# Optimization experiments

Measured on AMD Instinct MI355X. Metric: run time of the kernel, lower is better.

Reference implementation:

```python
import jax, jax.numpy as jnp
import numpy as np

B, S, D = 2, 1024, 4096          # batch, prefill seqlen, model dim
H, KVH, HD = 32, 8, 128          # q heads, kv heads, head dim
MAX = 2048                       # kv-cache capacity
THETA = 1000000.0
REP = H // KVH


def _rope_tables(pos):
    # pos: [S] int -> cos/sin [S, HD]
    inv_freq = 1.0 / (THETA ** (jnp.arange(0, HD, 2, dtype=jnp.float32) / HD))
    freqs = pos[:, None].astype(jnp.float32) * inv_freq[None, :]
    emb = jnp.concatenate([freqs, freqs], axis=-1)
    return jnp.cos(emb), jnp.sin(emb)


def _rotate_half(t):
    t1, t2 = jnp.split(t, 2, axis=-1)
    return jnp.concatenate([-t2, t1], axis=-1)


def setup_inputs() -> dict:
    key = jax.random.key(0)
    k = jax.random.split(key, 8)
    sc = 1.0 / np.sqrt(D)
    x = jax.random.normal(k[0], (B, S, D), jnp.float32)
    storage_idx = jnp.arange(S, dtype=jnp.int32)
    cache = jnp.zeros((2, 1, B, KVH, MAX, HD), jnp.float32)
    causal = jnp.tril(jnp.ones((MAX, MAX), bool))
    mask = jnp.where(causal, 0.0, -1e9).astype(jnp.float32)
    Wq = jax.random.normal(k[1], (D, H * HD), jnp.float32) * sc
    bq = jax.random.normal(k[2], (H * HD,), jnp.float32) * 0.01
    Wk = jax.random.normal(k[3], (D, KVH * HD), jnp.float32) * sc
    bk = jax.random.normal(k[4], (KVH * HD,), jnp.float32) * 0.01
    Wv = jax.random.normal(k[5], (D, KVH * HD), jnp.float32) * sc
    bv = jax.random.normal(k[6], (KVH * HD,), jnp.float32) * 0.01
    Wo = jax.random.normal(k[7], (H * HD, D), jnp.float32) * sc
    return {"x": x, "storage_idx": storage_idx, "cache": cache, "mask": mask,
            "Wq": Wq, "bq": bq, "Wk": Wk, "bk": bk, "Wv": Wv, "bv": bv, "Wo": Wo}


def reference(x, storage_idx, cache, mask, Wq, bq, Wk, bk, Wv, bv, Wo):
    bsz, seqlen, _ = x.shape
    # QKV projections -> [b, heads, s, hd]
    xq = (x @ Wq + bq).reshape(bsz, seqlen, H, HD).transpose(0, 2, 1, 3)
    xk = (x @ Wk + bk).reshape(bsz, seqlen, KVH, HD).transpose(0, 2, 1, 3)
    xv = (x @ Wv + bv).reshape(bsz, seqlen, KVH, HD).transpose(0, 2, 1, 3)
    # inline RoPE at positions storage_idx
    cos, sin = _rope_tables(storage_idx)       # [s, hd]
    cos = cos[None, None]                      # [1,1,s,hd]
    sin = sin[None, None]
    xq = xq * cos + _rotate_half(xq) * sin
    xk = xk * cos + _rotate_half(xk) * sin
    # KV-cache scatter (index_copy_ on dim -2 at storage_idx)
    keys = cache[0, 0].at[:, :, storage_idx, :].set(xk)    # [b, kvh, MAX, hd]
    values = cache[1, 0].at[:, :, storage_idx, :].set(xv)
    # GQA: repeat kv heads
    keys = jnp.repeat(keys, REP, axis=1)       # [b, H, MAX, hd]
    values = jnp.repeat(values, REP, axis=1)
    # attention with additive mask rows gathered at storage_idx
    scores = jnp.einsum('bhqd,bhkd->bhqk', xq, keys) / np.sqrt(HD)
    scores = scores + mask[storage_idx][None, None]        # [b, H, s, MAX]
    attn = jax.nn.softmax(scores, axis=-1)
    out = jnp.einsum('bhqk,bhkd->bhqd', attn, values)
    out = out.transpose(0, 2, 1, 3).reshape(bsz, seqlen, H * HD)
    return out @ Wo
```

## Files before the change

### kernel.cpp

```cpp
#include <hip/hip_runtime.h>
#include <hip/hip_bf16.h>

typedef unsigned short u16;
typedef unsigned int   u32;
using bf16x8 = __attribute__((ext_vector_type(8))) short;
using f32x4  = __attribute__((ext_vector_type(4))) float;

#define AS1 __attribute__((address_space(1)))
#define AS3 __attribute__((address_space(3)))

static constexpr int S_   = 1024;
static constexpr int D_   = 4096;
static constexpr int H_   = 32;
static constexpr int KVH_ = 8;
static constexpr int HD_  = 128;
static constexpr int NQKV = H_*HD_ + 2*KVH_*HD_;

__device__ __forceinline__ u16 f2bf(float f) {
  union { float f; u32 u; } v; v.f = f;
  u32 r = v.u + 0x7FFFu + ((v.u >> 16) & 1u);
  return (u16)(r >> 16);
}

__global__ void k_convert(const float* __restrict__ src, u16* __restrict__ dst, int n4) {
  int i = blockIdx.x * blockDim.x + threadIdx.x;
  if (i >= n4) return;
  float4 v = ((const float4*)src)[i];
  ushort4 o;
  o.x = f2bf(v.x); o.y = f2bf(v.y); o.z = f2bf(v.z); o.w = f2bf(v.w);
  ((ushort4*)dst)[i] = o;
}

__global__ __launch_bounds__(256) void k_transpose_w(
    const float* __restrict__ src, u16* __restrict__ dst, int K, int N) {
  __shared__ float t[64][65];
  int k0 = blockIdx.y * 64, n0 = blockIdx.x * 64;
  int tid = threadIdx.x;
  int lr = tid >> 4;
  int lc = (tid & 15) * 4;
#pragma unroll
  for (int i = 0; i < 4; ++i) {
    float4 v = *(const float4*)&src[(size_t)(k0 + lr + i*16) * N + n0 + lc];
    t[lc+0][lr + i*16] = v.x;
    t[lc+1][lr + i*16] = v.y;
    t[lc+2][lr + i*16] = v.z;
    t[lc+3][lr + i*16] = v.w;
  }
  __syncthreads();
  int wn = tid >> 3;
  int wk = (tid & 7) * 8;
#pragma unroll
  for (int i = 0; i < 2; ++i) {
    const float* row = &t[wn + i*32][wk];
    ushort4 a, b;
    a.x = f2bf(row[0]); a.y = f2bf(row[1]); a.z = f2bf(row[2]); a.w = f2bf(row[3]);
    b.x = f2bf(row[4]); b.y = f2bf(row[5]); b.z = f2bf(row[6]); b.w = f2bf(row[7]);
    u16* o = &dst[(size_t)(n0 + wn + i*32) * K + k0 + wk];
    *(ushort4*)o = a;
    *(ushort4*)(o + 4) = b;
  }
}

__global__ void k_transpose_v(const u16* __restrict__ src, u16* __restrict__ dst) {
  __shared__ u16 t[32][33];
  int bg = blockIdx.z;
  int s0 = blockIdx.x * 32, h0 = blockIdx.y * 32;
  src += (size_t)bg * S_ * HD_;
  dst += (size_t)bg * S_ * HD_;
  int tx = threadIdx.x, ty = threadIdx.y;
#pragma unroll
  for (int i = 0; i < 4; ++i)
    t[ty + i*8][tx] = src[(size_t)(s0 + ty + i*8) * HD_ + h0 + tx];
  __syncthreads();
#pragma unroll
  for (int i = 0; i < 4; ++i)
    dst[(size_t)(h0 + ty + i*8) * S_ + s0 + tx] = t[tx][ty + i*8];
}

__global__ void k_rope(const int* __restrict__ sidx, float* __restrict__ cosd,
                       float* __restrict__ sind) {
  int i = blockIdx.x * blockDim.x + threadIdx.x;
  int s = i >> 6, d = i & 63;
  float pos  = (float)sidx[s];
  float invf = expf(-0.21586735246819178f * (float)d);
  float ph   = pos * invf;
  cosd[i] = cosf(ph);
  sind[i] = sinf(ph);
}

#define BAR   __builtin_amdgcn_s_barrier()
#define SCHB  __builtin_amdgcn_sched_barrier(0)

__global__ __launch_bounds__(512, 2) void k_gemmq(
    const u16* __restrict__ A, const u16* __restrict__ Bt,
    const float* __restrict__ bq, const float* __restrict__ bk,
    const float* __restrict__ bv,
    const float* __restrict__ cosd, const float* __restrict__ sind,
    u16* __restrict__ qb, u16* __restrict__ kb, u16* __restrict__ vb)
{
  constexpr int K = 4096;
  constexpr int ABYT = 256*128, BBYT = 256*128, STEP = ABYT+BBYT;
  __shared__ __align__(16) char lds[2*STEP];

  const int cpx = (int)gridDim.x >> 3;
  const int wkid = ((int)blockIdx.x & 7)*cpx + ((int)blockIdx.x >> 3);
  const int NT = 24;
  const int m0 = (wkid / NT) * 256, n0 = (wkid % NT) * 256;
  const int tid = threadIdx.x, w = tid>>6, lane = tid&63;
  const int l15 = lane&15, l4 = lane>>4;
  const int wr = w>>1, wc = w&1;
  const int row0 = tid>>3;
  const int ss = (tid&7) ^ (row0&7);
  const int NK = K >> 6;

  f32x4 acc[4][8];
#pragma unroll
  for (int i = 0; i < 4; ++i)
#pragma unroll
    for (int j = 0; j < 8; ++j) acc[i][j] = (f32x4){0.f,0.f,0.f,0.f};

  bf16x8 af[2][2][2];
  bf16x8 bfr[2][4][2];

#define QCHUNK(kt_, part_, r0c_)                                              \
  __builtin_amdgcn_global_load_lds(                                           \
    (AS1 void*)(((part_) ? Bt + (size_t)(n0 + (r0c_) + row0)*K                \
                         : A  + (size_t)(m0 + (r0c_) + row0)*K)               \
                + (size_t)(kt_)*64 + ss*8),                                   \
    (AS3 void*)(lds + ((kt_)&1)*STEP + (part_)*ABYT + (r0c_)*128 + w*1024),   \
    16, 0, 0)

#define QR_A(mh_, lA_)                                                        \
  _Pragma("unroll") for (int i2 = 0; i2 < 2; ++i2)                            \
  _Pragma("unroll") for (int kk = 0; kk < 2; ++kk) {                          \
    int row = wr*64 + ((mh_)*2 + i2)*16 + l15;                                \
    af[mh_][i2][kk] = *(const bf16x8*)((lA_) + row*128 + (((kk*4+l4) ^ (row&7)) << 4)); }

#define QR_B(nh_, lB_)                                                        \
  _Pragma("unroll") for (int jj = 0; jj < 4; ++jj)                            \
  _Pragma("unroll") for (int kk = 0; kk < 2; ++kk) {                          \
    int row = wc*128 + ((nh_)*4 + jj)*16 + l15;                               \
    bfr[nh_][jj][kk] = *(const bf16x8*)((lB_) + row*128 + (((kk*4+l4) ^ (row&7)) << 4)); }

#define QMFMA(mh_, nh_)                                                       \
  __builtin_amdgcn_s_setprio(1);                                              \
  _Pragma("unroll") for (int i2 = 0; i2 < 2; ++i2)                            \
  _Pragma("unroll") for (int jj = 0; jj < 4; ++jj)                            \
  _Pragma("unroll") for (int kk = 0; kk < 2; ++kk)                            \
    acc[(mh_)*2+i2][(nh_)*4+jj] = __builtin_amdgcn_mfma_f32_16x16x32_bf16(    \
        af[mh_][i2][kk], bfr[nh_][jj][kk], acc[(mh_)*2+i2][(nh_)*4+jj], 0, 0, 0); \
  __builtin_amdgcn_s_setprio(0);

  QCHUNK(0,0,0); QCHUNK(0,0,64); QCHUNK(0,0,128); QCHUNK(0,0,192);
  QCHUNK(0,1,0); QCHUNK(0,1,64); QCHUNK(0,1,128); QCHUNK(0,1,192);
  QCHUNK(1,0,0); QCHUNK(1,0,64); QCHUNK(1,0,128); QCHUNK(1,0,192);
  QCHUNK(1,1,0); QCHUNK(1,1,64); QCHUNK(1,1,128); QCHUNK(1,1,192);
  asm volatile("s_waitcnt vmcnt(8)" ::: "memory");
  BAR; SCHB;
  {
    const char* lA0 = lds;
    const char* lB0 = lds + ABYT;
    QR_A(0, lA0); QR_B(0, lB0);
  }

  for (int kt = 0; kt < NK; ++kt) {
    const char* lA = lds + (kt&1)*STEP;
    const char* lB = lA + ABYT;
    QR_B(1, lB);
    asm volatile("s_waitcnt lgkmcnt(8)" ::: "memory");
    SCHB;
    QMFMA(0,0);
    QR_A(1, lA);
    asm volatile("s_waitcnt lgkmcnt(4)" ::: "memory");
    BAR; SCHB;
    if (kt+2 < NK) { QCHUNK(kt+2,1,0); QCHUNK(kt+2,1,64); QCHUNK(kt+2,1,128); QCHUNK(kt+2,1,192); }
    QMFMA(0,1);
    asm volatile("s_waitcnt lgkmcnt(0)" ::: "memory");
    BAR; SCHB;
    if (kt+2 < NK) { QCHUNK(kt+2,0,0); QCHUNK(kt+2,0,64); QCHUNK(kt+2,0,128); QCHUNK(kt+2,0,192); }
    QMFMA(1,0);
    if (kt+1 < NK) {
      if (kt+2 < NK) asm volatile("s_waitcnt vmcnt(8)" ::: "memory");
      else           asm volatile("s_waitcnt vmcnt(0)" ::: "memory");
      BAR; SCHB;
      const char* lAn = lds + ((kt+1)&1)*STEP;
      const char* lBn = lAn + ABYT;
      QR_A(0, lAn); QR_B(0, lBn);
      SCHB;
    }
    QMFMA(1,1);
  }
#undef QCHUNK
#undef QR_A
#undef QR_B
#undef QMFMA

  const int btype = (n0 >= H_*HD_) + (n0 >= H_*HD_ + KVH_*HD_);
  const int colbase = n0 + wc*128 - (btype==1 ? H_*HD_ : btype==2 ? H_*HD_+KVH_*HD_ : 0);
  const int hloc = colbase >> 7;
  const float* bias = btype==0 ? bq : btype==1 ? bk : bv;
  u16* dst = btype==0 ? qb : btype==1 ? kb : vb;
  const int nheads = btype==0 ? H_ : KVH_;
  const float scale = btype==0 ? 0.08838834764831845f : 1.0f;

  float bb[8];
#pragma unroll
  for (int j = 0; j < 8; ++j) bb[j] = bias[colbase + j*16 + l15];

#pragma unroll
  for (int i = 0; i < 4; ++i)
#pragma unroll
    for (int r = 0; r < 4; ++r) {
      int sr = m0 + wr*64 + i*16 + l4*4 + r;
      int b_ = sr >> 10, s_ = sr & 1023;
      size_t obase = (((size_t)b_*nheads + hloc)*S_ + s_)*(size_t)HD_;
      if (btype < 2) {
#pragma unroll
        for (int j = 0; j < 4; ++j) {
          float cs = cosd[s_*64 + j*16 + l15];
          float sn = sind[s_*64 + j*16 + l15];
          float lo = acc[i][j][r]   + bb[j];
          float hi = acc[i][j+4][r] + bb[j+4];
          dst[obase + j*16 + l15]      = f2bf((lo*cs - hi*sn) * scale);
          dst[obase + 64 + j*16 + l15] = f2bf((hi*cs + lo*sn) * scale);
        }
      } else {
#pragma unroll
        for (int j = 0; j < 8; ++j)
          dst[obase + j*16 + l15] = f2bf(acc[i][j][r] + bb[j]);
      }
    }
}

__global__ __launch_bounds__(512, 2) void k_gemmo(
    const u16* __restrict__ A, const u16* __restrict__ Bt,
    float* __restrict__ C, int N, int K)
{
  constexpr int ABYT = 128*128, BBYT = 256*128, STEP = ABYT+BBYT;
  __shared__ __align__(16) char lds[2*STEP];

  const int cpx = (int)gridDim.x >> 3;
  const int wkid = ((int)blockIdx.x & 7)*cpx + ((int)blockIdx.x >> 3);
  const int NT = N / 256;
  const int m0 = (wkid / NT) * 128, n0 = (wkid % NT) * 256;
  const int tid = threadIdx.x, w = tid>>6, lane = tid&63;
  const int l15 = lane&15, l4 = lane>>4;
  const int wr = w>>2, wc = w&3;
  const int row0 = tid>>3;
  const int ss = (tid&7) ^ (row0&7);
  const int NK = K >> 6;

  f32x4 acc[4][4];
#pragma unroll
  for (int i = 0; i < 4; ++i)
#pragma unroll
    for (int j = 0; j < 4; ++j) acc[i][j] = (f32x4){0.f,0.f,0.f,0.f};

  bf16x8 af[2][2][2];
  bf16x8 bfr[2][2][2];

#define OCHUNK(kt_, part_, r0c_)                                              \
  __builtin_amdgcn_global_load_lds(                                           \
    (AS1 void*)(((part_) ? Bt + (size_t)(n0 + (r0c_) + row0)*K                \
                         : A  + (size_t)(m0 + (r0c_) + row0)*K)               \
                + (size_t)(kt_)*64 + ss*8),                                   \
    (AS3 void*)(lds + ((kt_)&1)*STEP + (part_)*ABYT + (r0c_)*128 + w*1024),   \
    16, 0, 0)

#define OR_A(mh_, lA_)                                                        \
  _Pragma("unroll") for (int i2 = 0; i2 < 2; ++i2)                            \
  _Pragma("unroll") for (int kk = 0; kk < 2; ++kk) {                          \
    int row = wr*64 + ((mh_)*2 + i2)*16 + l15;                                \
    af[mh_][i2][kk] = *(const bf16x8*)((lA_) + row*128 + (((kk*4+l4) ^ (row&7)) << 4)); }

#define OR_B(nh_, lB_)                                                        \
  _Pragma("unroll") for (int j2 = 0; j2 < 2; ++j2)                            \
  _Pragma("unroll") for (int kk = 0; kk < 2; ++kk) {                          \
    int row = wc*64 + ((nh_)*2 + j2)*16 + l15;                                \
    bfr[nh_][j2][kk] = *(const bf16x8*)((lB_) + row*128 + (((kk*4+l4) ^ (row&7)) << 4)); }

#define OMFMA(mh_, nh_)                                                       \
  __builtin_amdgcn_s_setprio(1);                                              \
  _Pragma("unroll") for (int i2 = 0; i2 < 2; ++i2)                            \
  _Pragma("unroll") for (int j2 = 0; j2 < 2; ++j2)                            \
  _Pragma("unroll") for (int kk = 0; kk < 2; ++kk)                            \
    acc[(mh_)*2+i2][(nh_)*2+j2] = __builtin_amdgcn_mfma_f32_16x16x32_bf16(    \
        af[mh_][i2][kk], bfr[nh_][j2][kk], acc[(mh_)*2+i2][(nh_)*2+j2], 0, 0, 0); \
  __builtin_amdgcn_s_setprio(0);

  OCHUNK(0,0,0); OCHUNK(0,0,64);
  OCHUNK(0,1,0); OCHUNK(0,1,64); OCHUNK(0,1,128); OCHUNK(0,1,192);
  OCHUNK(1,0,0); OCHUNK(1,0,64);
  OCHUNK(1,1,0); OCHUNK(1,1,64); OCHUNK(1,1,128); OCHUNK(1,1,192);
  asm volatile("s_waitcnt vmcnt(6)" ::: "memory");
  BAR; SCHB;
  {
    const char* lA0 = lds;
    const char* lB0 = lds + ABYT;
    OR_A(0, lA0); OR_B(0, lB0);
  }

  for (int kt = 0; kt < NK; ++kt) {
    const char* lA = lds + (kt&1)*STEP;
    const char* lB = lA + ABYT;
    OR_B(1, lB);
    asm volatile("s_waitcnt lgkmcnt(4)" ::: "memory");
    SCHB;
    OMFMA(0,0);
    OR_A(1, lA);
    asm volatile("s_waitcnt lgkmcnt(4)" ::: "memory");
    BAR; SCHB;
    if (kt+2 < NK) { OCHUNK(kt+2,1,0); OCHUNK(kt+2,1,64); OCHUNK(kt+2,1,128); OCHUNK(kt+2,1,192); }
    OMFMA(0,1);
    asm volatile("s_waitcnt lgkmcnt(0)" ::: "memory");
    BAR; SCHB;
    if (kt+2 < NK) { OCHUNK(kt+2,0,0); OCHUNK(kt+2,0,64); }
    OMFMA(1,0);
    if (kt+1 < NK) {
      if (kt+2 < NK) asm volatile("s_waitcnt vmcnt(6)" ::: "memory");
      else           asm volatile("s_waitcnt vmcnt(0)" ::: "memory");
      BAR; SCHB;
      const char* lAn = lds + ((kt+1)&1)*STEP;
      const char* lBn = lAn + ABYT;
      OR_A(0, lAn); OR_B(0, lBn);
      SCHB;
    }
    OMFMA(1,1);
  }
#undef OCHUNK
#undef OR_A
#undef OR_B
#undef OMFMA

#pragma unroll
  for (int i = 0; i < 4; ++i)
#pragma unroll
    for (int j = 0; j < 4; ++j) {
      int r0 = m0 + wr*64 + i*16 + l4*4;
      int c0 = n0 + wc*64 + j*16 + l15;
#pragma unroll
      for (int r = 0; r < 4; ++r)
        C[(size_t)(r0 + r) * N + c0] = acc[i][j][r];
    }
}

__global__ __launch_bounds__(256, 4) void k_attn(
    const u16* __restrict__ Q, const u16* __restrict__ Kc,
    const u16* __restrict__ Vt, u16* __restrict__ AO)
{
  __shared__ __align__(16) char Kls[2][16384];
  __shared__ __align__(16) char Vls[2][16384];
  __shared__ u16 Pl[4][1024];

  int id = blockIdx.x;
  int slot = id >> 3;
  int bg   = (id & 7)*2 + (slot & 1);
  int rem  = slot >> 1;
  int h_in = rem & 3, bx = rem >> 2;
  int b = bg >> 3, g = bg & 7, h = g*4 + h_in;
  int tA = bx, tB = 15 - bx;

  int tid = threadIdx.x, w = tid >> 6, lane = tid & 63;
  int l15 = lane & 15, l4 = lane >> 4;
  const u16* Qh = Q  + ((size_t)b*H_   + h) * S_ * HD_;
  const u16* Kp = Kc + ((size_t)b*KVH_ + g) * S_ * HD_;
  const u16* Vp = Vt + ((size_t)b*KVH_ + g) * (size_t)HD_ * S_;
  u16* AOh = AO + ((size_t)b*S_) * (H_*HD_) + h*HD_;
  char* Pw = (char*)&Pl[w][0];

  int kOff[4], vOff[4];
#pragma unroll
  for (int c = 0; c < 4; ++c) {
    int ci = c*256 + tid;
    int krow = ci >> 4, ks = ci & 15;
    kOff[c] = krow * HD_ + ((ks & 8) | ((ks & 7) ^ (krow & 7))) * 8;
    int vrow = ci >> 3, vs = ci & 7;
    vOff[c] = vrow * S_ + (vs ^ (vrow & 7)) * 8;
  }

#define ASTAGE(kv_, bb_) {                                                    \
    const u16* ks_ = Kp + (size_t)(kv_) * 64 * HD_;                           \
    const u16* vs_ = Vp + (size_t)(kv_) * 64;                                 \
    _Pragma("unroll") for (int c = 0; c < 4; ++c) {                           \
      __builtin_amdgcn_global_load_lds((AS1 void*)(ks_ + kOff[c]),            \
          (AS3 void*)(&Kls[bb_][0] + c*4096 + w*1024), 16, 0, 0);             \
      __builtin_amdgcn_global_load_lds((AS1 void*)(vs_ + vOff[c]),            \
          (AS3 void*)(&Vls[bb_][0] + c*4096 + w*1024), 16, 0, 0); } }

  bf16x8 qf[4];
#pragma unroll
  for (int kc = 0; kc < 4; ++kc)
    qf[kc] = *(const bf16x8*)(Qh + (size_t)(tA*64 + w*16 + l15)*HD_ + kc*32 + l4*8);

  f32x4 o[8];
#pragma unroll
  for (int n = 0; n < 8; ++n) o[n] = (f32x4){0.f,0.f,0.f,0.f};
  float mrow[4] = {-3e38f,-3e38f,-3e38f,-3e38f};
  float lrow[4] = {0.f,0.f,0.f,0.f};

  ASTAGE(0, 0);
  asm volatile("s_waitcnt vmcnt(0)" ::: "memory");
  __builtin_amdgcn_s_barrier();

  const int NIT = tA + tB + 2;
  int buf = 0;
  for (int it = 0; it < NIT; ++it) {
    bool phA = (it <= tA);
    int kv = phA ? it : it - tA - 1;
    int qt = phA ? tA : tB;
    if (it + 1 < NIT) {
      int kvn = (it + 1 <= tA) ? it + 1 : it - tA;
      ASTAGE(kvn, buf ^ 1);
    }
    const char* Ksb = &Kls[buf][0];
    const char* Vsb = &Vls[buf][0];

    f32x4 sc[4];
    __builtin_amdgcn_s_setprio(1);
#pragma unroll
    for (int ct = 0; ct < 4; ++ct) {
      f32x4 s4 = (f32x4){0.f,0.f,0.f,0.f};
#pragma unroll
      for (int kc = 0; kc < 4; ++kc) {
        int row = ct*16 + l15, s = kc*4 + l4;
        bf16x8 kf = *(const bf16x8*)(Ksb + row*256 + ((((s & 7) ^ (row & 7)) | (s & 8)) << 4));
        s4 = __builtin_amdgcn_mfma_f32_16x16x32_bf16(qf[kc], kf, s4, 0, 0, 0);
      }
      sc[ct] = s4;
    }
    __builtin_amdgcn_s_setprio(0);

    if (kv == qt) {
      int qrow0 = qt*64 + w*16;
#pragma unroll
      for (int ct = 0; ct < 4; ++ct)
#pragma unroll
        for (int r = 0; r < 4; ++r) {
          int col = kv*64 + ct*16 + l15;
          if (col > qrow0 + l4*4 + r) sc[ct][r] = -1e9f;
        }
    }

    float f[4];
#pragma unroll
    for (int r = 0; r < 4; ++r) {
      float mx = fmaxf(fmaxf(sc[0][r], sc[1][r]), fmaxf(sc[2][r], sc[3][r]));
      mx = fmaxf(mx, __shfl_xor(mx, 1));
      mx = fmaxf(mx, __shfl_xor(mx, 2));
      mx = fmaxf(mx, __shfl_xor(mx, 4));
      mx = fmaxf(mx, __shfl_xor(mx, 8));
      float nm = fmaxf(mrow[r], mx);
      f[r] = __expf(mrow[r] - nm);
      mrow[r] = nm;
    }
    float rs[4] = {0.f,0.f,0.f,0.f};
#pragma unroll
    for (int ct = 0; ct < 4; ++ct)
#pragma unroll
      for (int r = 0; r < 4; ++r) {
        float p = __expf(sc[ct][r] - mrow[r]);
        rs[r] += p;
        int row = l4*4 + r, col = ct*16 + l15;
        int byte = row*128 + (((col >> 3) ^ (row & 7)) << 4) + (col & 7)*2;
        *(u16*)(Pw + byte) = f2bf(p);
      }
#pragma unroll
    for (int r = 0; r < 4; ++r) {
      float sum = rs[r];
      sum += __shfl_xor(sum, 1);
      sum += __shfl_xor(sum, 2);
      sum += __shfl_xor(sum, 4);
      sum += __shfl_xor(sum, 8);
      lrow[r] = lrow[r]*f[r] + sum;
    }
#pragma unroll
    for (int n = 0; n < 8; ++n)
#pragma unroll
      for (int r = 0; r < 4; ++r) o[n][r] *= f[r];

    __builtin_amdgcn_s_setprio(1);
#pragma unroll
    for (int kk = 0; kk < 2; ++kk) {
      int pbyte = l15*128 + (((kk*4 + l4) ^ (l15 & 7)) << 4);
      bf16x8 pf = *(const bf16x8*)(Pw + pbyte);
#pragma unroll
      for (int n = 0; n < 8; ++n) {
        int vrow = n*16 + l15, s = kk*4 + l4;
        bf16x8 vf = *(const bf16x8*)(Vsb + vrow*128 + ((s ^ (vrow & 7)) << 4));
        o[n] = __builtin_amdgcn_mfma_f32_16x16x32_bf16(pf, vf, o[n], 0, 0, 0);
      }
    }
    __builtin_amdgcn_s_setprio(0);

    if (it == tA) {
#pragma unroll
      for (int n = 0; n < 8; ++n)
#pragma unroll
        for (int r = 0; r < 4; ++r) {
          int srow = tA*64 + w*16 + l4*4 + r;
          AOh[(size_t)srow * (H_*HD_) + n*16 + l15] = f2bf(o[n][r] / lrow[r]);
        }
#pragma unroll
      for (int n = 0; n < 8; ++n) o[n] = (f32x4){0.f,0.f,0.f,0.f};
#pragma unroll
      for (int r = 0; r < 4; ++r) { mrow[r] = -3e38f; lrow[r] = 0.f; }
#pragma unroll
      for (int kc = 0; kc < 4; ++kc)
        qf[kc] = *(const bf16x8*)(Qh + (size_t)(tB*64 + w*16 + l15)*HD_ + kc*32 + l4*8);
    }

    asm volatile("s_waitcnt vmcnt(0)" ::: "memory");
    __builtin_amdgcn_s_barrier();
    buf ^= 1;
  }
#undef ASTAGE

#pragma unroll
  for (int n = 0; n < 8; ++n)
#pragma unroll
    for (int r = 0; r < 4; ++r) {
      int srow = tB*64 + w*16 + l4*4 + r;
      AOh[(size_t)srow * (H_*HD_) + n*16 + l15] = f2bf(o[n][r] / lrow[r]);
    }
}

extern "C" void kernel_launch(void* const* d_in, const int* in_sizes, int n_in,
                              void* d_out, int out_size, void* d_ws, size_t ws_size,
                              hipStream_t stream) {
  (void)in_sizes; (void)n_in; (void)out_size; (void)ws_size;
  const float* x   = (const float*)d_in[0];
  const int*   sid = (const int*)  d_in[1];
  const float* Wq  = (const float*)d_in[4];
  const float* bq  = (const float*)d_in[5];
  const float* Wk  = (const float*)d_in[6];
  const float* bk  = (const float*)d_in[7];
  const float* Wv  = (const float*)d_in[8];
  const float* bv  = (const float*)d_in[9];
  const float* Wo  = (const float*)d_in[10];
  float* out = (float*)d_out;

  char* ws = (char*)d_ws;
  u16*   xb   = (u16*)  (ws);
  u16*   WB   = (u16*)  (ws + 16777216);
  u16*   WoT  = (u16*)  (ws + 67108864);
  u16*   qb   = (u16*)  (ws + 150994944);
  u16*   kb   = (u16*)  (ws + 167772160);
  u16*   vb   = (u16*)  (ws + 171966464);
  u16*   VT   = (u16*)  (ws + 176160768);
  float* cosd = (float*)(ws + 180355072);
  float* sind = (float*)(ws + 180617216);
  u16*   AO   = xb;

  dim3 tb(32, 8);
  k_convert<<<8192, 256, 0, stream>>>(x, xb, (2048*4096)/4);
  k_transpose_w<<<dim3(64,64), 256, 0, stream>>>(Wq, WB, 4096, 4096);
  k_transpose_w<<<dim3(16,64), 256, 0, stream>>>(Wk, WB + (size_t)4096*4096, 4096, 1024);
  k_transpose_w<<<dim3(16,64), 256, 0, stream>>>(Wv, WB + (size_t)5120*4096, 4096, 1024);
  k_transpose_w<<<dim3(64,64), 256, 0, stream>>>(Wo, WoT, 4096, 4096);
  k_rope<<<256, 256, 0, stream>>>(sid, cosd, sind);
  k_gemmq<<<192, 512, 0, stream>>>(xb, WB, bq, bk, bv, cosd, sind, qb, kb, vb);
  k_transpose_v<<<dim3(32,4,16), tb, 0, stream>>>(vb, VT);
  k_attn<<<512, 256, 0, stream>>>(qb, kb, VT, AO);
  k_gemmo<<<256, 512, 0, stream>>>(AO, WoT, out, 4096, 4096);
}
```

Baseline: 286.4 us.

## Use 32x32x16 MFMA in output GEMM and merge weight transposes into one launch

The output projection GEMM switches from 16x16x32 bf16 MFMA tiles to 32x32x16 tiles. Each wave now holds four 32x32 accumulators instead of sixteen 16x16 ones, and the LDS fragment reads and output write indexing change to match. Separately, the four weight-transpose launches are merged into one kernel that routes by block index, which cuts launch overhead and tail gaps. The larger MFMA shape issues fewer instructions and reuses operands better, but it changes the LDS read pattern and could add bank conflicts or shift register pressure.

```diff
diff --git a/kernel.cpp b/kernel.cpp
--- a/kernel.cpp
+++ b/kernel.cpp
@@ -5,6 +5,7 @@
 typedef unsigned int   u32;
 using bf16x8 = __attribute__((ext_vector_type(8))) short;
 using f32x4  = __attribute__((ext_vector_type(4))) float;
+using f32x16 = __attribute__((ext_vector_type(16))) float;
 
 #define AS1 __attribute__((address_space(1)))
 #define AS3 __attribute__((address_space(3)))
@@ -31,10 +32,19 @@
   ((ushort4*)dst)[i] = o;
 }
 
-__global__ __launch_bounds__(256) void k_transpose_w(
-    const float* __restrict__ src, u16* __restrict__ dst, int K, int N) {
+__global__ __launch_bounds__(256) void k_transpose_all(
+    const float* __restrict__ Wq, const float* __restrict__ Wk,
+    const float* __restrict__ Wv, const float* __restrict__ Wo,
+    u16* __restrict__ WB, u16* __restrict__ WoT) {
+  constexpr int K = 4096;
   __shared__ float t[64][65];
-  int k0 = blockIdx.y * 64, n0 = blockIdx.x * 64;
+  int id = blockIdx.x;
+  const float* src; u16* dst; int N, tx, ty;
+  if (id < 4096)      { src = Wq; dst = WB;                        N = 4096; tx = id & 63; ty = id >> 6; }
+  else if (id < 5120) { id -= 4096; src = Wk; dst = WB + (size_t)4096*K; N = 1024; tx = id & 15; ty = id >> 4; }
+  else if (id < 6144) { id -= 5120; src = Wv; dst = WB + (size_t)5120*K; N = 1024; tx = id & 15; ty = id >> 4; }
+  else                { id -= 6144; src = Wo; dst = WoT;           N = 4096; tx = id & 63; ty = id >> 6; }
+  int k0 = ty * 64, n0 = tx * 64;
   int tid = threadIdx.x;
   int lr = tid >> 4;
   int lc = (tid & 15) * 4;
@@ -244,20 +254,16 @@
   const int NT = N / 256;
   const int m0 = (wkid / NT) * 128, n0 = (wkid % NT) * 256;
   const int tid = threadIdx.x, w = tid>>6, lane = tid&63;
-  const int l15 = lane&15, l4 = lane>>4;
+  const int l31 = lane & 31, lh = lane >> 5;
   const int wr = w>>2, wc = w&3;
   const int row0 = tid>>3;
   const int ss = (tid&7) ^ (row0&7);
   const int NK = K >> 6;
 
-  f32x4 acc[4][4];
-#pragma unroll
-  for (int i = 0; i < 4; ++i)
-#pragma unroll
-    for (int j = 0; j < 4; ++j) acc[i][j] = (f32x4){0.f,0.f,0.f,0.f};
-
-  bf16x8 af[2][2][2];
-  bf16x8 bfr[2][2][2];
+  f32x16 acc00 = {}, acc01 = {}, acc10 = {}, acc11 = {};
+
+  bf16x8 af[2][4];
+  bf16x8 bfr[2][4];
 
 #define OCHUNK(kt_, part_, r0c_)                                              \
   __builtin_amdgcn_global_load_lds(                                           \
@@ -268,24 +274,19 @@
     16, 0, 0)
 
 #define OR_A(mh_, lA_)                                                        \
-  _Pragma("unroll") for (int i2 = 0; i2 < 2; ++i2)                            \
-  _Pragma("unroll") for (int kk = 0; kk < 2; ++kk) {                          \
-    int row = wr*64 + ((mh_)*2 + i2)*16 + l15;                                \
-    af[mh_][i2][kk] = *(const bf16x8*)((lA_) + row*128 + (((kk*4+l4) ^ (row&7)) << 4)); }
+  _Pragma("unroll") for (int st = 0; st < 4; ++st) {                          \
+    int row = wr*64 + (mh_)*32 + l31;                                         \
+    af[mh_][st] = *(const bf16x8*)((lA_) + row*128 + ((((st*2)+lh) ^ (row&7)) << 4)); }
 
 #define OR_B(nh_, lB_)                                                        \
-  _Pragma("unroll") for (int j2 = 0; j2 < 2; ++j2)                            \
-  _Pragma("unroll") for (int kk = 0; kk < 2; ++kk) {                          \
-    int row = wc*64 + ((nh_)*2 + j2)*16 + l15;                                \
-    bfr[nh_][j2][kk] = *(const bf16x8*)((lB_) + row*128 + (((kk*4+l4) ^ (row&7)) << 4)); }
-
-#define OMFMA(mh_, nh_)                                                       \
+  _Pragma("unroll") for (int st = 0; st < 4; ++st) {                          \
+    int row = wc*64 + (nh_)*32 + l31;                                         \
+    bfr[nh_][st] = *(const bf16x8*)((lB_) + row*128 + ((((st*2)+lh) ^ (row&7)) << 4)); }
+
+#define OMFMA(mh_, nh_, accv_)                                                \
   __builtin_amdgcn_s_setprio(1);                                              \
-  _Pragma("unroll") for (int i2 = 0; i2 < 2; ++i2)                            \
-  _Pragma("unroll") for (int j2 = 0; j2 < 2; ++j2)                            \
-  _Pragma("unroll") for (int kk = 0; kk < 2; ++kk)                            \
-    acc[(mh_)*2+i2][(nh_)*2+j2] = __builtin_amdgcn_mfma_f32_16x16x32_bf16(    \
-        af[mh_][i2][kk], bfr[nh_][j2][kk], acc[(mh_)*2+i2][(nh_)*2+j2], 0, 0, 0); \
+  _Pragma("unroll") for (int st = 0; st < 4; ++st)                            \
+    accv_ = __builtin_amdgcn_mfma_f32_32x32x16_bf16(af[mh_][st], bfr[nh_][st], accv_, 0, 0, 0); \
   __builtin_amdgcn_s_setprio(0);
 
   OCHUNK(0,0,0); OCHUNK(0,0,64);
@@ -306,16 +307,16 @@
     OR_B(1, lB);
     asm volatile("s_waitcnt lgkmcnt(4)" ::: "memory");
     SCHB;
-    OMFMA(0,0);
+    OMFMA(0,0, acc00);
     OR_A(1, lA);
     asm volatile("s_waitcnt lgkmcnt(4)" ::: "memory");
     BAR; SCHB;
     if (kt+2 < NK) { OCHUNK(kt+2,1,0); OCHUNK(kt+2,1,64); OCHUNK(kt+2,1,128); OCHUNK(kt+2,1,192); }
-    OMFMA(0,1);
+    OMFMA(0,1, acc01);
     asm volatile("s_waitcnt lgkmcnt(0)" ::: "memory");
     BAR; SCHB;
     if (kt+2 < NK) { OCHUNK(kt+2,0,0); OCHUNK(kt+2,0,64); }
-    OMFMA(1,0);
+    OMFMA(1,0, acc10);
     if (kt+1 < NK) {
       if (kt+2 < NK) asm volatile("s_waitcnt vmcnt(6)" ::: "memory");
       else           asm volatile("s_waitcnt vmcnt(0)" ::: "memory");
@@ -325,23 +326,20 @@
       OR_A(0, lAn); OR_B(0, lBn);
       SCHB;
     }
-    OMFMA(1,1);
+    OMFMA(1,1, acc11);
   }
 #undef OCHUNK
 #undef OR_A
 #undef OR_B
 #undef OMFMA
 
-#pragma unroll
-  for (int i = 0; i < 4; ++i)
-#pragma unroll
-    for (int j = 0; j < 4; ++j) {
-      int r0 = m0 + wr*64 + i*16 + l4*4;
-      int c0 = n0 + wc*64 + j*16 + l15;
-#pragma unroll
-      for (int r = 0; r < 4; ++r)
-        C[(size_t)(r0 + r) * N + c0] = acc[i][j][r];
-    }
+#define OWRITE(mh_, nh_, accv_)                                               \
+  _Pragma("unroll") for (int r = 0; r < 16; ++r) {                            \
+    int row = m0 + wr*64 + (mh_)*32 + (r & 3) + 8*(r >> 2) + 4*lh;            \
+    int col = n0 + wc*64 + (nh_)*32 + l31;                                    \
+    C[(size_t)row * N + col] = accv_[r]; }
+  OWRITE(0,0, acc00); OWRITE(0,1, acc01); OWRITE(1,0, acc10); OWRITE(1,1, acc11);
+#undef OWRITE
 }
 
 __global__ __launch_bounds__(256, 4) void k_attn(
@@ -553,10 +551,7 @@
 
   dim3 tb(32, 8);
   k_convert<<<8192, 256, 0, stream>>>(x, xb, (2048*4096)/4);
-  k_transpose_w<<<dim3(64,64), 256, 0, stream>>>(Wq, WB, 4096, 4096);
-  k_transpose_w<<<dim3(16,64), 256, 0, stream>>>(Wk, WB + (size_t)4096*4096, 4096, 1024);
-  k_transpose_w<<<dim3(16,64), 256, 0, stream>>>(Wv, WB + (size_t)5120*4096, 4096, 1024);
-  k_transpose_w<<<dim3(64,64), 256, 0, stream>>>(Wo, WoT, 4096, 4096);
+  k_transpose_all<<<10240, 256, 0, stream>>>(Wq, Wk, Wv, Wo, WB, WoT);
   k_rope<<<256, 256, 0, stream>>>(sid, cosd, sind);
   k_gemmq<<<192, 512, 0, stream>>>(xb, WB, bq, bk, bv, cosd, sind, qb, kb, vb);
   k_transpose_v<<<dim3(32,4,16), tb, 0, stream>>>(vb, VT);
```

New measurement: 287.9 us. No clear change (+0.5%).
